# Kernel tuning notes

Measured on AMD Instinct MI355X. Metric: run time of the kernel, lower is better.

Reference implementation:

```python
import jax, jax.numpy as jnp
import numpy as np

EMBED_DIM = 768
NUM_HEADS = 12
HEAD_DIM = EMBED_DIM // NUM_HEADS
SCALE = HEAD_DIM ** -0.5


def setup_inputs() -> dict:
    key = jax.random.key(0)
    k_x, k_wqkv, k_bqkv, k_wfc, k_bfc = jax.random.split(key, 5)
    B, S, D = 32, 577, EMBED_DIM
    x = jax.random.normal(k_x, (B, S, D), dtype=jnp.float32)
    # torch Linear default init ~ U(-1/sqrt(fan_in), 1/sqrt(fan_in)); scale suffices
    lim = 1.0 / np.sqrt(D)
    w_qkv = jax.random.uniform(k_wqkv, (D, 3 * D), jnp.float32, -lim, lim)
    b_qkv = jax.random.uniform(k_bqkv, (3 * D,), jnp.float32, -lim, lim)
    w_fc = jax.random.uniform(k_wfc, (D, D), jnp.float32, -lim, lim)
    b_fc = jax.random.uniform(k_bfc, (D,), jnp.float32, -lim, lim)
    return {"x": x, "w_qkv": w_qkv, "b_qkv": b_qkv, "w_fc": w_fc, "b_fc": b_fc}


def reference(x, w_qkv, b_qkv, w_fc, b_fc):
    B, S, D = x.shape
    H, Dh = NUM_HEADS, HEAD_DIM
    qkv = x @ w_qkv + b_qkv                      # [B,S,3D]
    qkv = qkv.reshape(B, S, 3, H, Dh)
    q, k, v = jnp.moveaxis(qkv, 2, 0)            # each [B,S,H,Dh]
    # scores: [B,H,S,S]
    attn = jnp.einsum('bqhd,bkhd->bhqk', q, k) * SCALE
    attn = jax.nn.softmax(attn, axis=-1)
    out = jnp.einsum('bhqk,bkhd->bqhd', attn, v).reshape(B, S, D)
    # dropout in eval mode -> identity
    return out @ w_fc + b_fc
```

## Files before the change

kernel.cpp:

```cpp
#include <hip/hip_runtime.h>
#include <hip/hip_bf16.h>
#include <stdint.h>

typedef __attribute__((ext_vector_type(8))) short short8;
typedef __attribute__((ext_vector_type(4))) float f32x4;

typedef __attribute__((address_space(3))) uint8_t lds_u8;
typedef __attribute__((address_space(1))) uint8_t glb_u8;

__device__ __forceinline__ void load_lds_16(const void* g, void* l) {
    __builtin_amdgcn_global_load_lds((glb_u8*)g, (lds_u8*)l, 16, 0, 0);
}

__device__ __forceinline__ unsigned short f2b(float f) {
    __hip_bfloat16 h = __float2bfloat16(f);
    return __builtin_bit_cast(unsigned short, h);
}
__device__ __forceinline__ ushort2 f2b2(float a, float b) {
    __hip_bfloat162 h = __float22bfloat162_rn(float2{a, b});
    ushort2 r;
    __builtin_memcpy(&r, &h, sizeof(r));
    return r;
}

constexpr int Bz = 32, Ss = 577, Dd = 768, Hh = 12;
constexpr int Mm = Bz * Ss;
constexpr int QKV_N = 3 * Dd;
constexpr float SCALE_L2E = 0.125f * 1.4426950408889634f;

__global__ void cast_f32_bf16(const float* __restrict__ src,
                              unsigned short* __restrict__ dst, int n4) {
    int i = blockIdx.x * blockDim.x + threadIdx.x;
    if (i >= n4) return;
    float4 v = ((const float4*)src)[i];
    ushort4 o;
    o.x = f2b(v.x); o.y = f2b(v.y); o.z = f2b(v.z); o.w = f2b(v.w);
    ((ushort4*)dst)[i] = o;
}

__global__ void transpose_cast(const float* __restrict__ src,
                               unsigned short* __restrict__ dst, int R, int C) {
    __shared__ unsigned short tile[32][33];
    int c0 = blockIdx.x * 32, r0 = blockIdx.y * 32;
    int tx = threadIdx.x, ty = threadIdx.y;
#pragma unroll
    for (int i = 0; i < 4; ++i)
        tile[ty + i * 8][tx] = f2b(src[(size_t)(r0 + ty + i * 8) * C + c0 + tx]);
    __syncthreads();
#pragma unroll
    for (int i = 0; i < 4; ++i) {
        int rr = ty + i * 8;
        dst[(size_t)(c0 + rr) * R + r0 + tx] = tile[tx][rr];
    }
}

template <int N_, bool OUT_BF16>
__global__ __launch_bounds__(256)
void gemm_tn(const unsigned short* __restrict__ A,
             const unsigned short* __restrict__ Bt,
             const float* __restrict__ bias,
             void* __restrict__ Cout) {
    constexpr int K = 768;
    constexpr int KB = K / 32;
    __shared__ __align__(16) uint8_t smem[32768];

    const int tid = threadIdx.x;
    const int wave = tid >> 6, lane = tid & 63;
    const int quad = lane >> 4, lc = lane & 15;
    const int wm = wave >> 1, wn = wave & 1;
    const int tm = blockIdx.x * 128;
    const int tn = blockIdx.y * 128;

    const int l4 = lane >> 2;
    const int cx = (lane & 3) ^ (l4 & 3);

    auto stage = [&](int kb, int buf) {
        uint8_t* Ab = smem + buf * 8192;
        uint8_t* Bb = smem + 16384 + buf * 8192;
#pragma unroll
        for (int i = 0; i < 2; ++i) {
            int lrow = wave * 32 + i * 16 + l4;
            int arow = tm + lrow; if (arow >= Mm) arow = Mm - 1;
            load_lds_16(A + (size_t)arow * K + kb * 32 + cx * 8,
                        (void*)(Ab + (wave * 32 + i * 16) * 64));
            int brow = tn + lrow;
            load_lds_16(Bt + (size_t)brow * K + kb * 32 + cx * 8,
                        (void*)(Bb + (wave * 32 + i * 16) * 64));
        }
    };

    f32x4 acc[4][4] = {};
    stage(0, 0);
    __syncthreads();

    for (int kb = 0; kb < KB; ++kb) {
        const int buf = kb & 1;
        if (kb + 1 < KB) stage(kb + 1, buf ^ 1);

        const unsigned short* Ar = (const unsigned short*)(smem + buf * 8192);
        const unsigned short* Br = (const unsigned short*)(smem + 16384 + buf * 8192);
        short8 af[4], bf[4];
#pragma unroll
        for (int i = 0; i < 4; ++i) {
            int row = wm * 64 + i * 16 + lc;
            int c = quad ^ (row & 3);
            af[i] = *(const short8*)(Ar + row * 32 + c * 8);
            int brow = wn * 64 + i * 16 + lc;
            int cb = quad ^ (brow & 3);
            bf[i] = *(const short8*)(Br + brow * 32 + cb * 8);
        }
#pragma unroll
        for (int i = 0; i < 4; ++i)
#pragma unroll
            for (int j = 0; j < 4; ++j)
                acc[i][j] = __builtin_amdgcn_mfma_f32_16x16x32_bf16(af[i], bf[j], acc[i][j], 0, 0, 0);
        __syncthreads();
    }

    float bv[4];
#pragma unroll
    for (int j = 0; j < 4; ++j) bv[j] = bias[tn + wn * 64 + j * 16 + lc];

    float* ep = (float*)smem + wave * (16 * 68);
    const int erow = lane >> 2, ec = (lane & 3) * 16;
#pragma unroll
    for (int i = 0; i < 4; ++i) {
#pragma unroll
        for (int j = 0; j < 4; ++j)
#pragma unroll
            for (int r = 0; r < 4; ++r)
                ep[(quad * 4 + r) * 68 + j * 16 + lc] = acc[i][j][r] + bv[j];
        __threadfence_block();
        int grow = tm + wm * 64 + i * 16 + erow;
        if (grow < Mm) {
            float4 c0 = *(float4*)&ep[erow * 68 + ec + 0];
            float4 c1 = *(float4*)&ep[erow * 68 + ec + 4];
            float4 c2 = *(float4*)&ep[erow * 68 + ec + 8];
            float4 c3 = *(float4*)&ep[erow * 68 + ec + 12];
            int gcol = tn + wn * 64 + ec;
            if constexpr (OUT_BF16) {
                unsigned short o[16];
                *(ushort2*)&o[0]  = f2b2(c0.x, c0.y);
                *(ushort2*)&o[2]  = f2b2(c0.z, c0.w);
                *(ushort2*)&o[4]  = f2b2(c1.x, c1.y);
                *(ushort2*)&o[6]  = f2b2(c1.z, c1.w);
                *(ushort2*)&o[8]  = f2b2(c2.x, c2.y);
                *(ushort2*)&o[10] = f2b2(c2.z, c2.w);
                *(ushort2*)&o[12] = f2b2(c3.x, c3.y);
                *(ushort2*)&o[14] = f2b2(c3.z, c3.w);
                unsigned short* op = (unsigned short*)Cout + (size_t)grow * N_ + gcol;
                *(short8*)(op + 0) = *(short8*)&o[0];
                *(short8*)(op + 8) = *(short8*)&o[8];
            } else {
                float* op = (float*)Cout + (size_t)grow * N_ + gcol;
                *(float4*)(op + 0)  = c0;
                *(float4*)(op + 4)  = c1;
                *(float4*)(op + 8)  = c2;
                *(float4*)(op + 12) = c3;
            }
        }
        __threadfence_block();
    }
}


template <bool TAIL>
__device__ __forceinline__ void attn_tile(
    const unsigned short* __restrict__ Ktile,
    const unsigned short* __restrict__ Vtb,
    unsigned short* __restrict__ Pqw,
    const short8& qf0, const short8& qf1,
    int quad, int lc,
    float& mrun, float& lrun, f32x4 (&oacc)[4]) {

    const int sw = lc & 7;
    f32x4 sfr[4];
#pragma unroll
    for (int f = 0; f < 4; ++f) {
        const unsigned short* kr = Ktile + (f * 16 + lc) * 64;
        short8 k0 = *(const short8*)(kr + (quad ^ sw) * 8);
        short8 k1 = *(const short8*)(kr + ((quad ^ 4) ^ sw) * 8);
        f32x4 z = {};
        z = __builtin_amdgcn_mfma_f32_16x16x32_bf16(k0, qf0, z, 0, 0, 0);
        z = __builtin_amdgcn_mfma_f32_16x16x32_bf16(k1, qf1, z, 0, 0, 0);
        sfr[f] = z;
    }

    float tv[4][4];
#pragma unroll
    for (int f = 0; f < 4; ++f)
#pragma unroll
        for (int r = 0; r < 4; ++r) {
            float s = sfr[f][r];
            if (TAIL && !(f == 0 && r == 0 && quad == 0)) s = -1e30f;
            tv[f][r] = s;
        }

    float m0 = tv[0][0];
#pragma unroll
    for (int f = 0; f < 4; ++f)
#pragma unroll
        for (int r = 0; r < 4; ++r) m0 = fmaxf(m0, tv[f][r]);
    m0 = fmaxf(m0, __shfl_xor(m0, 16, 64));
    m0 = fmaxf(m0, __shfl_xor(m0, 32, 64));
    float mnew = fmaxf(mrun, m0);
    float mc = mnew * SCALE_L2E;
    float alpha = exp2f(__builtin_fmaf(mrun, SCALE_L2E, -mc));
    mrun = mnew;

    float sum = 0.f;
#pragma unroll
    for (int f = 0; f < 4; ++f) {
        float p0 = exp2f(__builtin_fmaf(tv[f][0], SCALE_L2E, -mc));
        float p1 = exp2f(__builtin_fmaf(tv[f][1], SCALE_L2E, -mc));
        float p2 = exp2f(__builtin_fmaf(tv[f][2], SCALE_L2E, -mc));
        float p3 = exp2f(__builtin_fmaf(tv[f][3], SCALE_L2E, -mc));
        sum += (p0 + p1) + (p2 + p3);
        ushort2 lo = f2b2(p0, p1), hi = f2b2(p2, p3);
        ushort4 pk = {lo.x, lo.y, hi.x, hi.y};
        *(ushort4*)&Pqw[lc * 72 + f * 16 + quad * 4] = pk;
    }
    sum += __shfl_xor(sum, 16, 64);
    sum += __shfl_xor(sum, 32, 64);
    lrun = lrun * alpha + sum;

#pragma unroll
    for (int g = 0; g < 4; ++g)
#pragma unroll
        for (int r = 0; r < 4; ++r) oacc[g][r] *= alpha;

    __threadfence_block();

    short8 pf0 = *(const short8*)&Pqw[lc * 72 + quad * 8];
    short8 pf1 = *(const short8*)&Pqw[lc * 72 + 32 + quad * 8];
#pragma unroll
    for (int g = 0; g < 4; ++g) {
        short8 vf0 = *(const short8*)&Vtb[(g * 16 + lc) * 80 + quad * 8];
        short8 vf1 = *(const short8*)&Vtb[(g * 16 + lc) * 80 + 32 + quad * 8];
        oacc[g] = __builtin_amdgcn_mfma_f32_16x16x32_bf16(vf0, pf0, oacc[g], 0, 0, 0);
        oacc[g] = __builtin_amdgcn_mfma_f32_16x16x32_bf16(vf1, pf1, oacc[g], 0, 0, 0);
    }
}

__global__ __launch_bounds__(512)
void attn_kernel(const unsigned short* __restrict__ qkv,
                 unsigned short* __restrict__ outb) {
    __shared__ unsigned short Kt[2][64 * 64];
    __shared__ unsigned short Vt[2][64 * 80];
    __shared__ unsigned short Pq[8][16 * 72];

    const int tid = threadIdx.x;
    const int wave = tid >> 6, lane = tid & 63;
    const int quad = lane >> 4, lc = lane & 15;
    const int qt = blockIdx.x, h = blockIdx.y, b = blockIdx.z;

    const unsigned short* qkvK = qkv + (size_t)b * Ss * QKV_N + h * 64 + 768;
    const unsigned short* qkvV = qkvK + 768;

    const int krow = lane >> 3;
    const int gch = (lane & 7) ^ krow;

    const int qbase = qt * 128 + wave * 16;
    int qrow = qbase + lc; if (qrow > Ss - 1) qrow = Ss - 1;
    const unsigned short* qp = qkv + (size_t)(b * Ss + qrow) * QKV_N + h * 64;
    short8 qf0 = *(const short8*)(qp + quad * 8);
    short8 qf1 = *(const short8*)(qp + 32 + quad * 8);

    unsigned short* Pqw = Pq[wave];

    auto stage_K = [&](int tile, int buf) {
        int key = tile * 64 + wave * 8 + krow; if (key > Ss - 1) key = Ss - 1;
        const unsigned short* gp = qkvK + (size_t)key * QKV_N + gch * 8;
        load_lds_16(gp, (void*)&Kt[buf][wave * 512]);
    };
    auto load_V = [&](int tile) -> short8 {
        int key = tile * 64 + lane; if (key > Ss - 1) key = Ss - 1;
        return *(const short8*)(qkvV + (size_t)key * QKV_N + wave * 8);
    };
    auto write_V = [&](short8 v, int buf) {
#pragma unroll
        for (int j = 0; j < 8; ++j)
            Vt[buf][(wave * 8 + j) * 80 + lane] = (unsigned short)v[j];
    };

    float mrun = -1e30f, lrun = 0.f;
    f32x4 oacc[4] = {};

    stage_K(0, 0);
    write_V(load_V(0), 0);
    __syncthreads();

    for (int kb = 0; kb < 9; ++kb) {
        const int buf = kb & 1;
        stage_K(kb + 1, buf ^ 1);
        short8 vreg = load_V(kb + 1);
        attn_tile<false>(Kt[buf], Vt[buf], Pqw, qf0, qf1, quad, lc, mrun, lrun, oacc);
        write_V(vreg, buf ^ 1);
        __syncthreads();
    }
    attn_tile<true>(Kt[1], Vt[1], Pqw, qf0, qf1, quad, lc, mrun, lrun, oacc);

    float inv = 1.f / lrun;
#pragma unroll
    for (int g = 0; g < 4; ++g) {
        ushort2 lo = f2b2(oacc[g][0] * inv, oacc[g][1] * inv);
        ushort2 hi = f2b2(oacc[g][2] * inv, oacc[g][3] * inv);
        ushort4 ob = {lo.x, lo.y, hi.x, hi.y};
        *(ushort4*)&Pqw[lc * 72 + g * 16 + quad * 4] = ob;
    }
    __threadfence_block();
#pragma unroll
    for (int p = 0; p < 2; ++p) {
        int lr = p * 8 + (lane >> 3), ch = lane & 7;
        int q = qbase + lr;
        if (q <= Ss - 1) {
            short8 vv = *(const short8*)&Pqw[lr * 72 + ch * 8];
            *(short8*)(outb + (size_t)(b * Ss + q) * Dd + h * 64 + ch * 8) = vv;
        }
    }
}

extern "C" void kernel_launch(void* const* d_in, const int* in_sizes, int n_in,
                              void* d_out, int out_size, void* d_ws, size_t ws_size,
                              hipStream_t stream) {
    const float* x     = (const float*)d_in[0];
    const float* w_qkv = (const float*)d_in[1];
    const float* b_qkv = (const float*)d_in[2];
    const float* w_fc  = (const float*)d_in[3];
    const float* b_fc  = (const float*)d_in[4];

    uint8_t* ws = (uint8_t*)d_ws;
    unsigned short* xb    = (unsigned short*)(ws + 0);
    unsigned short* wqkvT = (unsigned short*)(ws + 28360704);
    unsigned short* wfcT  = (unsigned short*)(ws + 31899648);
    unsigned short* qkv   = (unsigned short*)(ws + 33079296);
    unsigned short* attn  = (unsigned short*)(ws + 118161408);

    int n4 = (Mm * Dd) / 4;
    cast_f32_bf16<<<(n4 + 255) / 256, 256, 0, stream>>>(x, xb, n4);
    transpose_cast<<<dim3(QKV_N / 32, Dd / 32), dim3(32, 8), 0, stream>>>(w_qkv, wqkvT, Dd, QKV_N);
    transpose_cast<<<dim3(Dd / 32, Dd / 32), dim3(32, 8), 0, stream>>>(w_fc, wfcT, Dd, Dd);

    gemm_tn<QKV_N, true><<<dim3((Mm + 127) / 128, QKV_N / 128), 256, 0, stream>>>(xb, wqkvT, b_qkv, qkv);

    attn_kernel<<<dim3(5, Hh, Bz), 512, 0, stream>>>(qkv, attn);

    gemm_tn<Dd, false><<<dim3((Mm + 127) / 128, Dd / 128), 256, 0, stream>>>(attn, wfcT, b_fc, d_out);
}
```

Before: 368.9 us.

## Replace direct-to-LDS loads with register-staged prefetch two stages ahead

The GEMM mainloop stops issuing global_load_lds copies and instead loads tiles into registers two k-blocks ahead, then writes them to swizzled LDS after compute. The loop is unrolled by two with fixed buffers. The goal is to hide global latency better and lift occupancy via launch_bounds(256,3). In exchange it uses more VGPRs for staging and adds explicit LDS store instructions.

```diff
diff --git a/kernel.cpp b/kernel.cpp
--- a/kernel.cpp
+++ b/kernel.cpp
@@ -54,8 +54,10 @@
     }
 }
 
+struct StageRegs { short8 a0, a1, b0, b1; };
+
 template <int N_, bool OUT_BF16>
-__global__ __launch_bounds__(256)
+__global__ __launch_bounds__(256, 3)
 void gemm_tn(const unsigned short* __restrict__ A,
              const unsigned short* __restrict__ Bt,
              const float* __restrict__ bias,
@@ -71,32 +73,33 @@
     const int tm = blockIdx.x * 128;
     const int tn = blockIdx.y * 128;
 
-    const int l4 = lane >> 2;
-    const int cx = (lane & 3) ^ (l4 & 3);
-
-    auto stage = [&](int kb, int buf) {
-        uint8_t* Ab = smem + buf * 8192;
-        uint8_t* Bb = smem + 16384 + buf * 8192;
-#pragma unroll
-        for (int i = 0; i < 2; ++i) {
-            int lrow = wave * 32 + i * 16 + l4;
-            int arow = tm + lrow; if (arow >= Mm) arow = Mm - 1;
-            load_lds_16(A + (size_t)arow * K + kb * 32 + cx * 8,
-                        (void*)(Ab + (wave * 32 + i * 16) * 64));
-            int brow = tn + lrow;
-            load_lds_16(Bt + (size_t)brow * K + kb * 32 + cx * 8,
-                        (void*)(Bb + (wave * 32 + i * 16) * 64));
-        }
+    const int srow = tid >> 1;
+    const int sc0 = (tid & 1) * 2;
+    int arow = tm + srow; if (arow >= Mm) arow = Mm - 1;
+    const unsigned short* gAr = A + (size_t)arow * K + sc0 * 8;
+    const unsigned short* gBr = Bt + (size_t)(tn + srow) * K + sc0 * 8;
+    const int wc0 = (sc0 ^ (srow & 3)) * 8;
+    const int wc1 = ((sc0 + 1) ^ (srow & 3)) * 8;
+
+    auto ld = [&](int kb) {
+        StageRegs r;
+        r.a0 = *(const short8*)(gAr + kb * 32);
+        r.a1 = *(const short8*)(gAr + kb * 32 + 8);
+        r.b0 = *(const short8*)(gBr + kb * 32);
+        r.b1 = *(const short8*)(gBr + kb * 32 + 8);
+        return r;
+    };
+    auto st = [&](const StageRegs& r, int buf) {
+        unsigned short* a = (unsigned short*)(smem + buf * 8192) + srow * 32;
+        unsigned short* b = (unsigned short*)(smem + 16384 + buf * 8192) + srow * 32;
+        *(short8*)(a + wc0) = r.a0;
+        *(short8*)(a + wc1) = r.a1;
+        *(short8*)(b + wc0) = r.b0;
+        *(short8*)(b + wc1) = r.b1;
     };
 
     f32x4 acc[4][4] = {};
-    stage(0, 0);
-    __syncthreads();
-
-    for (int kb = 0; kb < KB; ++kb) {
-        const int buf = kb & 1;
-        if (kb + 1 < KB) stage(kb + 1, buf ^ 1);
-
+    auto compute = [&](int buf) {
         const unsigned short* Ar = (const unsigned short*)(smem + buf * 8192);
         const unsigned short* Br = (const unsigned short*)(smem + 16384 + buf * 8192);
         short8 af[4], bf[4];
@@ -114,6 +117,21 @@
 #pragma unroll
             for (int j = 0; j < 4; ++j)
                 acc[i][j] = __builtin_amdgcn_mfma_f32_16x16x32_bf16(af[i], bf[j], acc[i][j], 0, 0, 0);
+    };
+
+    StageRegs r1 = ld(1);
+    StageRegs r0 = ld(0);
+    st(r0, 0);
+    __syncthreads();
+
+    for (int kb = 0; kb < KB; kb += 2) {
+        StageRegs rn = ld(kb + 2 < KB ? kb + 2 : KB - 1);
+        compute(0);
+        st(r1, 1);
+        __syncthreads();
+        r1 = ld(kb + 3 < KB ? kb + 3 : KB - 1);
+        compute(1);
+        st(rn, 0);
         __syncthreads();
     }
 
```

After: 394.2 us. 6.9% more time.
